# Kernel optimization log

Hardware: AMD Instinct MI355X
Metric: run time of the kernel (lower is better)

## Reference

```python
import jax, jax.numpy as jnp
import numpy as np

B, T, C, H, L, V = 512, 128, 512, 8, 6, 13
D = C // H  # 64


def setup_inputs() -> dict:
    key = jax.random.key(0)
    ks = jax.random.split(key, 12)
    s = 0.02
    return {
        "token_idxs": jax.random.randint(ks[0], (B, T), 0, V),
        "label": jax.random.randint(ks[1], (B,), 0, V),
        "wte": jax.random.normal(ks[2], (V, C), jnp.float32) * s,
        "wpe": jax.random.normal(ks[3], (T, C), jnp.float32) * s,
        "Wq": jax.random.normal(ks[4], (L, C, C), jnp.float32) * s,
        "bq": jnp.zeros((L, C), jnp.float32),
        "Wk": jax.random.normal(ks[5], (L, C, C), jnp.float32) * s,
        "bk": jnp.zeros((L, C), jnp.float32),
        "Wv": jax.random.normal(ks[6], (L, C, C), jnp.float32) * s,
        "bv": jnp.zeros((L, C), jnp.float32),
        "Wo": jax.random.normal(ks[7], (L, C, C), jnp.float32) * s,
        "bo": jnp.zeros((L, C), jnp.float32),
        "ln_g": jnp.ones((L, C), jnp.float32),
        "ln_b": jnp.zeros((L, C), jnp.float32),
        "W_lm": jax.random.normal(ks[8], (C, V), jnp.float32) * s,
        "b_lm": jnp.zeros((V,), jnp.float32),
    }


def _layer_norm(x, g, b, eps=1e-5):
    m = jnp.mean(x, axis=-1, keepdims=True)
    v = jnp.var(x, axis=-1, keepdims=True)
    return (x - m) / jnp.sqrt(v + eps) * g + b


def reference(token_idxs, label, wte, wpe, Wq, bq, Wk, bk, Wv, bv, Wo, bo, ln_g, ln_b, W_lm, b_lm):
    b, t = token_idxs.shape
    x = wte[token_idxs] + wpe[jnp.arange(t)]  # [b,t,C]
    inv_sqrt_d = 1.0 / jnp.sqrt(jnp.float32(D))
    for i in range(L):
        q = (x @ Wq[i] + bq[i]).reshape(b, t, H, D)
        k = (x @ Wk[i] + bk[i]).reshape(b, t, H, D)
        v = (x @ Wv[i] + bv[i]).reshape(b, t, H, D)
        # NOTE: matches the source exactly: attention over the HEAD axis at
        # each (b,t) position -> att shape [b,t,H,H]
        att = jnp.einsum('bthd,btgd->bthg', q, k) * inv_sqrt_d
        att = jax.nn.softmax(att, axis=-1)
        hid = jnp.einsum('bthg,btgd->bthd', att, v).reshape(b, t, C)
        x = _layer_norm(hid @ Wo[i] + bo[i] + x, ln_g[i], ln_b[i])
    logits = x @ W_lm + b_lm  # [b,t,V]
    logp = jax.nn.log_softmax(logits[:, -1, :], axis=-1)
    loss = -jnp.take_along_axis(logp, label[:, None], axis=-1).mean()
    return logits, loss
```

## Files before the change

kernel.cpp:

```cpp
#include <hip/hip_runtime.h>
#include <hip/hip_bf16.h>
#include <cstdint>
#include <cstddef>


typedef __attribute__((ext_vector_type(8))) short short8;
typedef __attribute__((ext_vector_type(4))) float f32x4;

__device__ __forceinline__ float bf2f(ushort u) {
    return __uint_as_float(((unsigned int)u) << 16);
}
__device__ __forceinline__ ushort f2bf(float f) {
    unsigned int x = __float_as_uint(f);
    unsigned int r = (x + 0x7fffu + ((x >> 16) & 1u)) >> 16;
    return (ushort)r;
}
__device__ __forceinline__ void gload_lds16(const void* g, void* l) {
    __builtin_amdgcn_global_load_lds(
        (const __attribute__((address_space(1))) void*)g,
        (__attribute__((address_space(3))) void*)l, 16, 0, 0);
}

__global__ __launch_bounds__(256) void prep_all(
    const float* __restrict__ Wq, const float* __restrict__ Wk,
    const float* __restrict__ Wv, const float* __restrict__ Wo,
    const float* __restrict__ wte, const float* __restrict__ wpe,
    const float* __restrict__ ln_g, const float* __restrict__ ln_b,
    ushort* __restrict__ wqkvT, ushort* __restrict__ woT,
    ushort* __restrict__ tmp0, float* __restrict__ s_qkv,
    float* __restrict__ t_qkv, float* __restrict__ psA,
    float* __restrict__ pssA, float* __restrict__ ones,
    float* __restrict__ zeros) {
    __shared__ float lds[64][65];
    __shared__ float gld[64], bld[64];
    __shared__ float sred[4][64], tred[4][64];
    const int bid = blockIdx.x;
    const int tid = threadIdx.x;
    if (bid < 192) {
        const int mat = bid >> 3;
        const int tc = bid & 7;
        const int l = mat >> 2, which = mat & 3;
        const float* S;
        switch (which) {
            case 0: S = Wq; break;
            case 1: S = Wk; break;
            case 2: S = Wv; break;
            default: S = Wo; break;
        }
        S += (size_t)l * 262144;
        ushort* T = (which < 3) ? wqkvT + (size_t)l * 786432 + which * 262144
                                : woT + (size_t)l * 262144;
        const bool fold = (which < 3);
        const float* g = (fold && l > 0) ? ln_g + (l - 1) * 512 : nullptr;
        const float* b = (fold && l > 0) ? ln_b + (l - 1) * 512 : nullptr;
        const int c = tid & 63;
        float sp = 0.f, tp = 0.f;
        for (int tr = 0; tr < 8; tr++) {
            __syncthreads();
            #pragma unroll
            for (int it = 0; it < 16; it++) {
                int r = it * 4 + (tid >> 6);
                lds[r][c] = S[(size_t)(tr * 64 + r) * 512 + tc * 64 + c];
            }
            if (tid < 64) {
                gld[tid] = g ? g[tr * 64 + tid] : 1.f;
                bld[tid] = b ? b[tr * 64 + tid] : 0.f;
            }
            __syncthreads();
            float gk = fold ? gld[c] : 1.f;
            #pragma unroll
            for (int it = 0; it < 16; it++) {
                int rn = it * 4 + (tid >> 6);
                float val = lds[c][rn] * gk;
                T[(size_t)(tc * 64 + rn) * 512 + tr * 64 + c] = f2bf(val);
            }
            if (fold) {
                #pragma unroll
                for (int i = 0; i < 16; i++) {
                    int kl = (tid >> 6) * 16 + i;
                    float w = lds[kl][c];
                    sp += gld[kl] * w;
                    tp += bld[kl] * w;
                }
            }
        }
        if (fold) {
            __syncthreads();
            sred[tid >> 6][c] = sp;
            tred[tid >> 6][c] = tp;
            __syncthreads();
            if (tid < 64) {
                float ss = sred[0][tid] + sred[1][tid] + sred[2][tid] + sred[3][tid];
                float tt = tred[0][tid] + tred[1][tid] + tred[2][tid] + tred[3][tid];
                int o = l * 1536 + which * 512 + tc * 64 + tid;
                s_qkv[o] = ss;
                t_qkv[o] = tt;
            }
        }
    } else if (bid < 608) {
        size_t idx = (size_t)(bid - 192) * 256 + tid;
        size_t u = idx >> 6;
        int c8 = (int)(idx & 63);
        int v = (int)(u >> 7);
        int t = (int)(u & 127);
        const float* ep = wte + (size_t)v * 512 + c8 * 8;
        const float* pp = wpe + (size_t)t * 512 + c8 * 8;
        float4 e0 = *(const float4*)ep, e1 = *(const float4*)(ep + 4);
        float4 p0 = *(const float4*)pp, p1 = *(const float4*)(pp + 4);
        float s[8] = {e0.x + p0.x, e0.y + p0.y, e0.z + p0.z, e0.w + p0.w,
                      e1.x + p1.x, e1.y + p1.y, e1.z + p1.z, e1.w + p1.w};
        short8 o;
        #pragma unroll
        for (int j = 0; j < 8; j++) o[j] = (short)f2bf(s[j]);
        *(short8*)(tmp0 + u * 512 + c8 * 8) = o;
    } else if (bid < 660) {
        int i = (bid - 608) * 256 + tid;
        if (i < 6656) psA[i] = 0.f;
        else {
            int j = i - 6656;
            pssA[j] = (j < 1664) ? 511.99488f : 0.f;
        }
    } else {
        ones[tid] = 1.f;  ones[tid + 256] = 1.f;
        zeros[tid] = 0.f; zeros[tid + 256] = 0.f;
    }
}

__global__ __launch_bounds__(256) void qkv_fold(
    const ushort* __restrict__ A, const float* __restrict__ psin,
    const float* __restrict__ pssin, const ushort* __restrict__ Bt,
    const float* __restrict__ s_l, const float* __restrict__ t_l,
    const float* __restrict__ b0, const float* __restrict__ b1,
    const float* __restrict__ b2, ushort* __restrict__ obf) {
    __shared__ alignas(16) ushort As[2][32 * 64];
    __shared__ alignas(16) ushort Bs[2][128 * 64];
    __shared__ float smu[32], srs[32];
    const int tid = threadIdx.x;
    const int lane = tid & 63;
    const int wave = tid >> 6;
    const int m0 = blockIdx.x * 32;
    const int n0 = blockIdx.y * 128;
    const int wm = (wave >> 1) * 16;
    const int wn = (wave & 1) * 64;
    const int r = lane & 15;
    const int kq = (lane >> 4) * 8;
    const ushort* Ab = A  + (size_t)m0 * 512;
    const ushort* Bb = Bt + (size_t)n0 * 512;
    f32x4 acc[4] = {};

    auto stage = [&](int t, int b) {
        const ushort* At = Ab + t * 64;
        const ushort* Bt2 = Bb + t * 64;
        {
            int cb = wave * 64;
            int ch = cb + lane;
            int row = ch >> 3;
            int c8 = (ch & 7) ^ (row & 7);
            gload_lds16(At + (size_t)row * 512 + c8 * 8, (char*)As[b] + cb * 16);
        }
        #pragma unroll
        for (int i = 0; i < 4; i++) {
            int cb = (i * 4 + wave) * 64;
            int ch = cb + lane;
            int row = ch >> 3;
            int c8 = (ch & 7) ^ (row & 7);
            gload_lds16(Bt2 + (size_t)row * 512 + c8 * 8, (char*)Bs[b] + cb * 16);
        }
    };

    stage(0, 0);
    if (tid < 32) {
        int row = m0 + tid;
        float s  = psin[row] + psin[1664 + row] + psin[3328 + row] + psin[4992 + row];
        float ss = pssin[row] + pssin[1664 + row] + pssin[3328 + row] + pssin[4992 + row];
        float mean = s * (1.f / 512.f);
        float var = ss * (1.f / 512.f) - mean * mean;
        smu[tid] = mean;
        srs[tid] = rsqrtf(var + 1e-5f);
    }
    __syncthreads();
    #pragma unroll
    for (int t = 0; t < 8; t++) {
        const int cur = t & 1;
        if (t < 7) stage(t + 1, cur ^ 1);
        #pragma unroll
        for (int kk = 0; kk < 64; kk += 32) {
            int arow = wm + r;
            int aoff = (arow * 128 + (kk + kq) * 2) ^ ((arow & 7) << 4);
            short8 af = *(const short8*)((const char*)As[cur] + aoff);
            #pragma unroll
            for (int n = 0; n < 4; n++) {
                int brow = wn + n * 16 + r;
                int boff = (brow * 128 + (kk + kq) * 2) ^ ((brow & 7) << 4);
                short8 bfr = *(const short8*)((const char*)Bs[cur] + boff);
                acc[n] = __builtin_amdgcn_mfma_f32_16x16x32_bf16(
                    af, bfr, acc[n], 0, 0, 0);
            }
        }
        __syncthreads();
    }
    const int r4 = (lane >> 4) * 4;
    const int cc = lane & 15;
    #pragma unroll
    for (int n = 0; n < 4; n++) {
        int cg = n0 + wn + n * 16 + cc;
        float bias = (cg < 512) ? b0[cg] : (cg < 1024) ? b1[cg - 512] : b2[cg - 1024];
        float sc = s_l[cg];
        float tc_ = t_l[cg] + bias;
        #pragma unroll
        for (int i = 0; i < 4; i++) {
            int lrow = wm + r4 + i;
            float v = srs[lrow] * (acc[n][i] - smu[lrow] * sc) + tc_;
            obf[(size_t)(m0 + lrow) * 1536 + cg] = f2bf(v);
        }
    }
}

__global__ __launch_bounds__(256) void attn_kernel(const ushort* __restrict__ qkv,
                                                   ushort* __restrict__ hid) {
    const int lane = threadIdx.x & 63;
    const size_t pos = (size_t)blockIdx.x * 4 + (threadIdx.x >> 6);
    const ushort* base = qkv + pos * 1536;
    const int h = lane >> 3, g = lane & 7;
    const ushort* qp = base + h * 64;
    const ushort* kp = base + 512 + g * 64;
    float s = 0.f;
    #pragma unroll
    for (int dc = 0; dc < 8; dc++) {
        short8 q8 = *(const short8*)(qp + dc * 8);
        short8 k8 = *(const short8*)(kp + dc * 8);
        #pragma unroll
        for (int j = 0; j < 8; j++) s += bf2f((ushort)q8[j]) * bf2f((ushort)k8[j]);
    }
    s *= 0.125f;
    float mx = s;
    #pragma unroll
    for (int o = 1; o < 8; o <<= 1) mx = fmaxf(mx, __shfl_xor(mx, o));
    float e = __expf(s - mx);
    float den = e;
    #pragma unroll
    for (int o = 1; o < 8; o <<= 1) den += __shfl_xor(den, o);
    float att = e / den;
    float o8[8];
    #pragma unroll
    for (int j = 0; j < 8; j++) o8[j] = 0.f;
    const ushort* vp = base + 1024 + (lane & 7) * 8;
    #pragma unroll
    for (int gg = 0; gg < 8; gg++) {
        float a = __shfl(att, (lane & 56) | gg);
        short8 v8 = *(const short8*)(vp + gg * 64);
        #pragma unroll
        for (int j = 0; j < 8; j++) o8[j] += a * bf2f((ushort)v8[j]);
    }
    short8 ov;
    #pragma unroll
    for (int j = 0; j < 8; j++) ov[j] = (short)f2bf(o8[j]);
    *(short8*)(hid + pos * 512 + lane * 8) = ov;
}

__global__ __launch_bounds__(256) void proj_fold(
    const ushort* __restrict__ A, const ushort* __restrict__ Bt,
    const float* __restrict__ bo_, const float* __restrict__ psin,
    const float* __restrict__ pssin, const float* __restrict__ g_in,
    const float* __restrict__ b_in, ushort* tmp,
    float* __restrict__ psout, float* __restrict__ pssout) {
    __shared__ alignas(16) ushort As[2][32 * 64];
    __shared__ alignas(16) ushort Bs[2][128 * 64];
    __shared__ float lps[2][32], lpss[2][32];
    __shared__ float smu[32], srs[32];
    const int tid = threadIdx.x;
    const int lane = tid & 63;
    const int wave = tid >> 6;
    const int m0 = blockIdx.x * 32;
    const int n0 = blockIdx.y * 128;
    const int wm = (wave >> 1) * 16;
    const int wn = (wave & 1) * 64;
    const int r = lane & 15;
    const int kq = (lane >> 4) * 8;
    const ushort* Ab = A  + (size_t)m0 * 512;
    const ushort* Bb = Bt + (size_t)n0 * 512;
    f32x4 acc[4] = {};

    auto stage = [&](int t, int b) {
        const ushort* At = Ab + t * 64;
        const ushort* Bt2 = Bb + t * 64;
        {
            int cb = wave * 64;
            int ch = cb + lane;
            int row = ch >> 3;
            int c8 = (ch & 7) ^ (row & 7);
            gload_lds16(At + (size_t)row * 512 + c8 * 8, (char*)As[b] + cb * 16);
        }
        #pragma unroll
        for (int i = 0; i < 4; i++) {
            int cb = (i * 4 + wave) * 64;
            int ch = cb + lane;
            int row = ch >> 3;
            int c8 = (ch & 7) ^ (row & 7);
            gload_lds16(Bt2 + (size_t)row * 512 + c8 * 8, (char*)Bs[b] + cb * 16);
        }
    };

    stage(0, 0);
    if (tid < 32) {
        int row = m0 + tid;
        float s  = psin[row] + psin[1664 + row] + psin[3328 + row] + psin[4992 + row];
        float ss = pssin[row] + pssin[1664 + row] + pssin[3328 + row] + pssin[4992 + row];
        float mean = s * (1.f / 512.f);
        float var = ss * (1.f / 512.f) - mean * mean;
        smu[tid] = mean;
        srs[tid] = rsqrtf(var + 1e-5f);
    }
    __syncthreads();
    #pragma unroll
    for (int t = 0; t < 8; t++) {
        const int cur = t & 1;
        if (t < 7) stage(t + 1, cur ^ 1);
        #pragma unroll
        for (int kk = 0; kk < 64; kk += 32) {
            int arow = wm + r;
            int aoff = (arow * 128 + (kk + kq) * 2) ^ ((arow & 7) << 4);
            short8 af = *(const short8*)((const char*)As[cur] + aoff);
            #pragma unroll
            for (int n = 0; n < 4; n++) {
                int brow = wn + n * 16 + r;
                int boff = (brow * 128 + (kk + kq) * 2) ^ ((brow & 7) << 4);
                short8 bfr = *(const short8*)((const char*)Bs[cur] + boff);
                acc[n] = __builtin_amdgcn_mfma_f32_16x16x32_bf16(
                    af, bfr, acc[n], 0, 0, 0);
            }
        }
        __syncthreads();
    }

    const int r4 = (lane >> 4) * 4;
    const int cc = lane & 15;
    float s_i[4] = {0.f, 0.f, 0.f, 0.f}, ss_i[4] = {0.f, 0.f, 0.f, 0.f};
    #pragma unroll
    for (int n = 0; n < 4; n++) {
        int col = n0 + wn + n * 16 + cc;
        float boc = bo_[col];
        float gc = g_in[col], bc = b_in[col];
        #pragma unroll
        for (int i = 0; i < 4; i++) {
            int lr = wm + r4 + i;
            int rg = m0 + lr;
            float resid = (bf2f(tmp[(size_t)rg * 512 + col]) - smu[lr])
                          * srs[lr] * gc + bc;
            float v = acc[n][i] + boc + resid;
            tmp[(size_t)rg * 512 + col] = f2bf(v);
            s_i[i] += v; ss_i[i] += v * v;
        }
    }
    #pragma unroll
    for (int i = 0; i < 4; i++) {
        #pragma unroll
        for (int o = 1; o < 16; o <<= 1) {
            s_i[i] += __shfl_xor(s_i[i], o);
            ss_i[i] += __shfl_xor(ss_i[i], o);
        }
    }
    if (cc == 0) {
        #pragma unroll
        for (int i = 0; i < 4; i++) {
            lps[wn >> 6][wm + r4 + i] = s_i[i];
            lpss[wn >> 6][wm + r4 + i] = ss_i[i];
        }
    }
    __syncthreads();
    if (tid < 32) {
        int row = m0 + tid;
        psout[blockIdx.y * 1664 + row]  = lps[0][tid] + lps[1][tid];
        pssout[blockIdx.y * 1664 + row] = lpss[0][tid] + lpss[1][tid];
    }
}

__global__ __launch_bounds__(256) void logits_ln(
    const ushort* __restrict__ tin, const float* __restrict__ psin,
    const float* __restrict__ pssin, const float* __restrict__ gv,
    const float* __restrict__ bv, const float* __restrict__ Wlm,
    const float* __restrict__ blm, float* __restrict__ lu) {
    __shared__ float wl[8 * 64 * 13];
    const int tid = threadIdx.x;
    for (int k = tid; k < 512; k += 256) {
        int dst = ((k & 7) * 64 + (k >> 3)) * 13;
        #pragma unroll
        for (int v = 0; v < 13; v++) wl[dst + v] = Wlm[k * 13 + v];
    }
    __syncthreads();
    const int lane = tid & 63;
    const int w = tid >> 6;
    const int c0 = lane * 8;
    float4 g0 = *(const float4*)(gv + c0), g1 = *(const float4*)(gv + c0 + 4);
    float4 b0 = *(const float4*)(bv + c0), b1 = *(const float4*)(bv + c0 + 4);
    float gg[8] = {g0.x, g0.y, g0.z, g0.w, g1.x, g1.y, g1.z, g1.w};
    float bb[8] = {b0.x, b0.y, b0.z, b0.w, b1.x, b1.y, b1.z, b1.w};
    float bl[13];
    #pragma unroll
    for (int v = 0; v < 13; v++) bl[v] = blm[v];
    for (int it = 0; it < 8; it++) {
        size_t row = (size_t)blockIdx.x * 32 + it * 4 + w;
        float s  = psin[row] + psin[1664 + row] + psin[3328 + row] + psin[4992 + row];
        float ss = pssin[row] + pssin[1664 + row] + pssin[3328 + row] + pssin[4992 + row];
        float mean = s * (1.f / 512.f);
        float rstd = rsqrtf(ss * (1.f / 512.f) - mean * mean + 1e-5f);
        short8 xv = *(const short8*)(tin + row * 512 + c0);
        float p[13];
        #pragma unroll
        for (int v = 0; v < 13; v++) p[v] = 0.f;
        #pragma unroll
        for (int j = 0; j < 8; j++) {
            float xf = (bf2f((ushort)xv[j]) - mean) * rstd * gg[j] + bb[j];
            const float* wr = wl + (j * 64 + lane) * 13;
            #pragma unroll
            for (int v = 0; v < 13; v++) p[v] += xf * wr[v];
        }
        #pragma unroll
        for (int v = 0; v < 13; v++) {
            #pragma unroll
            for (int o = 32; o > 0; o >>= 1) p[v] += __shfl_xor(p[v], o);
        }
        if (lane == 0) {
            #pragma unroll
            for (int v = 0; v < 13; v++) lu[row * 13 + v] = p[v] + bl[v];
        }
    }
}

__global__ __launch_bounds__(256) void scatter_loss(
    const float* __restrict__ lu, const int* __restrict__ tok,
    const int* __restrict__ label, float* __restrict__ out) {
    __shared__ float red[4];
    const int tid = threadIdx.x;
    if (blockIdx.x < 3328) {
        unsigned int i = blockIdx.x * 256 + tid;
        unsigned int bt = i / 13u;
        unsigned int vv = i - bt * 13u;
        int v = tok[bt];
        int t = (int)(bt & 127u);
        out[i] = lu[(size_t)((v << 7) + t) * 13 + vv];
    } else {
        float acc = 0.f;
        for (int b = tid; b < 512; b += 256) {
            int v = tok[b * 128 + 127];
            const float* lg = lu + (size_t)((v << 7) + 127) * 13;
            float mx = lg[0];
            #pragma unroll
            for (int vv = 1; vv < 13; vv++) mx = fmaxf(mx, lg[vv]);
            float den = 0.f;
            #pragma unroll
            for (int vv = 0; vv < 13; vv++) den += expf(lg[vv] - mx);
            int lab = label[b];
            acc += -(lg[lab] - mx - logf(den));
        }
        #pragma unroll
        for (int o = 32; o > 0; o >>= 1) acc += __shfl_xor(acc, o);
        if ((tid & 63) == 0) red[tid >> 6] = acc;
        __syncthreads();
        if (tid == 0)
            out[851968] = (red[0] + red[1] + red[2] + red[3]) * (1.f / 512.f);
    }
}

extern "C" void kernel_launch(void* const* d_in, const int* in_sizes, int n_in,
                              void* d_out, int out_size, void* d_ws, size_t ws_size,
                              hipStream_t stream) {
    const int*   tok   = (const int*)d_in[0];
    const int*   label = (const int*)d_in[1];
    const float* wte   = (const float*)d_in[2];
    const float* wpe   = (const float*)d_in[3];
    const float* Wq    = (const float*)d_in[4];
    const float* bq    = (const float*)d_in[5];
    const float* Wk    = (const float*)d_in[6];
    const float* bk    = (const float*)d_in[7];
    const float* Wv    = (const float*)d_in[8];
    const float* bv    = (const float*)d_in[9];
    const float* Wo    = (const float*)d_in[10];
    const float* bo    = (const float*)d_in[11];
    const float* ln_g  = (const float*)d_in[12];
    const float* ln_b  = (const float*)d_in[13];
    const float* Wlm   = (const float*)d_in[14];
    const float* blm   = (const float*)d_in[15];
    float* out = (float*)d_out;

    char* ws = (char*)d_ws;
    ushort* wqkvT = (ushort*)(ws);
    ushort* woT   = (ushort*)(ws + 9437184);
    ushort* qkv_u = (ushort*)(ws + 12582912);
    ushort* hid_u = (ushort*)(ws + 17694720);
    ushort* tmp   = (ushort*)(ws + 19398656);
    float*  psA   = (float*) (ws + 21102592);
    float*  pssA  = (float*) (ws + 21129216);
    float*  psB   = (float*) (ws + 21155840);
    float*  pssB  = (float*) (ws + 21182464);
    float*  lu    = (float*) (ws + 21209088);
    float*  s_qkv = (float*) (ws + 21295616);
    float*  t_qkv = (float*) (ws + 21332480);
    float*  ones  = (float*) (ws + 21369344);
    float*  zeros = (float*) (ws + 21371392);

    prep_all<<<661, 256, 0, stream>>>(Wq, Wk, Wv, Wo, wte, wpe, ln_g, ln_b,
                                      wqkvT, woT, tmp, s_qkv, t_qkv,
                                      psA, pssA, ones, zeros);

    const float *psin = psA, *pssin = pssA;
    float *psout = psB, *pssout = pssB;
    for (int l = 0; l < 6; l++) {
        const float* g_in = (l == 0) ? ones  : ln_g + (l - 1) * 512;
        const float* b_in = (l == 0) ? zeros : ln_b + (l - 1) * 512;
        qkv_fold<<<dim3(52, 12), 256, 0, stream>>>(
            tmp, psin, pssin, wqkvT + (size_t)l * 786432,
            s_qkv + l * 1536, t_qkv + l * 1536,
            bq + l * 512, bk + l * 512, bv + l * 512, qkv_u);
        attn_kernel<<<416, 256, 0, stream>>>(qkv_u, hid_u);
        proj_fold<<<dim3(52, 4), 256, 0, stream>>>(
            hid_u, woT + (size_t)l * 262144, bo + l * 512,
            psin, pssin, g_in, b_in, tmp, psout, pssout);
        const float* p1 = psin;  psin = psout;  psout = (float*)p1;
        const float* p2 = pssin; pssin = pssout; pssout = (float*)p2;
    }

    logits_ln<<<52, 256, 0, stream>>>(tmp, psin, pssin,
                                      ln_g + 5 * 512, ln_b + 5 * 512, Wlm, blm, lu);
    scatter_loss<<<3329, 256, 0, stream>>>(lu, tok, label, out);
}
```

Measured before the change: 221.5 us.

## Split weight prep into per-tile transpose blocks and separate fold-reduction blocks

The prep kernel previously had 192 blocks, each looping over 8 row-tiles to transpose a 64-column strip while also accumulating the LayerNorm fold sums. It now launches one block per 64x64 tile for the transpose (1536 blocks) and a separate set of 144 blocks that read the weights directly to compute the s/t fold vectors. The goal is to expose far more parallelism in the prep phase and cut its serial latency. The cost is that the fold blocks re-read the fp32 weights from global memory with strided loads, and the block-index ranges are reordered.

```diff
diff --git a/kernel.cpp b/kernel.cpp
--- a/kernel.cpp
+++ b/kernel.cpp
@@ -31,14 +31,13 @@
     float* __restrict__ t_qkv, float* __restrict__ psA,
     float* __restrict__ pssA, float* __restrict__ ones,
     float* __restrict__ zeros) {
-    __shared__ float lds[64][65];
-    __shared__ float gld[64], bld[64];
-    __shared__ float sred[4][64], tred[4][64];
     const int bid = blockIdx.x;
     const int tid = threadIdx.x;
-    if (bid < 192) {
-        const int mat = bid >> 3;
-        const int tc = bid & 7;
+    if (bid < 1536) {
+        __shared__ float lds[64][65];
+        const int mat = bid >> 6;
+        const int tile = bid & 63;
+        const int tr = tile >> 3, tc = tile & 7;
         const int l = mat >> 2, which = mat & 3;
         const float* S;
         switch (which) {
@@ -50,55 +49,53 @@
         S += (size_t)l * 262144;
         ushort* T = (which < 3) ? wqkvT + (size_t)l * 786432 + which * 262144
                                 : woT + (size_t)l * 262144;
-        const bool fold = (which < 3);
-        const float* g = (fold && l > 0) ? ln_g + (l - 1) * 512 : nullptr;
-        const float* b = (fold && l > 0) ? ln_b + (l - 1) * 512 : nullptr;
         const int c = tid & 63;
+        #pragma unroll
+        for (int it = 0; it < 16; it++) {
+            int r = it * 4 + (tid >> 6);
+            lds[r][c] = S[(size_t)(tr * 64 + r) * 512 + tc * 64 + c];
+        }
+        float gk = 1.f;
+        if (which < 3 && l > 0) gk = ln_g[(l - 1) * 512 + tr * 64 + c];
+        __syncthreads();
+        #pragma unroll
+        for (int it = 0; it < 16; it++) {
+            int r = it * 4 + (tid >> 6);
+            T[(size_t)(tc * 64 + r) * 512 + tr * 64 + c] = f2bf(lds[c][r] * gk);
+        }
+    } else if (bid < 1680) {
+        __shared__ float sred[4][64], tred[4][64];
+        const int j = bid - 1536;
+        const int mat = j >> 3;
+        const int tc = j & 7;
+        const int l = mat / 3, which = mat % 3;
+        const float* S = (which == 0) ? Wq : (which == 1) ? Wk : Wv;
+        S += (size_t)l * 262144;
+        const float* g = (l > 0) ? ln_g + (l - 1) * 512 : nullptr;
+        const float* b = (l > 0) ? ln_b + (l - 1) * 512 : nullptr;
+        const int c = tid & 63;
+        const int kc = tid >> 6;
         float sp = 0.f, tp = 0.f;
-        for (int tr = 0; tr < 8; tr++) {
-            __syncthreads();
-            #pragma unroll
-            for (int it = 0; it < 16; it++) {
-                int r = it * 4 + (tid >> 6);
-                lds[r][c] = S[(size_t)(tr * 64 + r) * 512 + tc * 64 + c];
-            }
-            if (tid < 64) {
-                gld[tid] = g ? g[tr * 64 + tid] : 1.f;
-                bld[tid] = b ? b[tr * 64 + tid] : 0.f;
-            }
-            __syncthreads();
-            float gk = fold ? gld[c] : 1.f;
-            #pragma unroll
-            for (int it = 0; it < 16; it++) {
-                int rn = it * 4 + (tid >> 6);
-                float val = lds[c][rn] * gk;
-                T[(size_t)(tc * 64 + rn) * 512 + tr * 64 + c] = f2bf(val);
-            }
-            if (fold) {
-                #pragma unroll
-                for (int i = 0; i < 16; i++) {
-                    int kl = (tid >> 6) * 16 + i;
-                    float w = lds[kl][c];
-                    sp += gld[kl] * w;
-                    tp += bld[kl] * w;
-                }
-            }
-        }
-        if (fold) {
-            __syncthreads();
-            sred[tid >> 6][c] = sp;
-            tred[tid >> 6][c] = tp;
-            __syncthreads();
-            if (tid < 64) {
-                float ss = sred[0][tid] + sred[1][tid] + sred[2][tid] + sred[3][tid];
-                float tt = tred[0][tid] + tred[1][tid] + tred[2][tid] + tred[3][tid];
-                int o = l * 1536 + which * 512 + tc * 64 + tid;
-                s_qkv[o] = ss;
-                t_qkv[o] = tt;
-            }
-        }
-    } else if (bid < 608) {
-        size_t idx = (size_t)(bid - 192) * 256 + tid;
+        for (int ki = 0; ki < 128; ki++) {
+            int k = kc * 128 + ki;
+            float w = S[(size_t)k * 512 + tc * 64 + c];
+            float gv = g ? g[k] : 1.f;
+            float bv = b ? b[k] : 0.f;
+            sp += gv * w;
+            tp += bv * w;
+        }
+        sred[kc][c] = sp;
+        tred[kc][c] = tp;
+        __syncthreads();
+        if (tid < 64) {
+            float ss = sred[0][tid] + sred[1][tid] + sred[2][tid] + sred[3][tid];
+            float tt = tred[0][tid] + tred[1][tid] + tred[2][tid] + tred[3][tid];
+            int o = l * 1536 + which * 512 + tc * 64 + tid;
+            s_qkv[o] = ss;
+            t_qkv[o] = tt;
+        }
+    } else if (bid < 2096) {
+        size_t idx = (size_t)(bid - 1680) * 256 + tid;
         size_t u = idx >> 6;
         int c8 = (int)(idx & 63);
         int v = (int)(u >> 7);
@@ -113,16 +110,16 @@
         #pragma unroll
         for (int j = 0; j < 8; j++) o[j] = (short)f2bf(s[j]);
         *(short8*)(tmp0 + u * 512 + c8 * 8) = o;
-    } else if (bid < 660) {
-        int i = (bid - 608) * 256 + tid;
+    } else if (bid == 2096) {
+        ones[tid] = 1.f;  ones[tid + 256] = 1.f;
+        zeros[tid] = 0.f; zeros[tid + 256] = 0.f;
+    } else {
+        int i = (bid - 2097) * 256 + tid;
         if (i < 6656) psA[i] = 0.f;
         else {
             int j = i - 6656;
             pssA[j] = (j < 1664) ? 511.99488f : 0.f;
         }
-    } else {
-        ones[tid] = 1.f;  ones[tid + 256] = 1.f;
-        zeros[tid] = 0.f; zeros[tid + 256] = 0.f;
     }
 }
 
@@ -499,9 +496,9 @@
     float*  ones  = (float*) (ws + 21369344);
     float*  zeros = (float*) (ws + 21371392);
 
-    prep_all<<<661, 256, 0, stream>>>(Wq, Wk, Wv, Wo, wte, wpe, ln_g, ln_b,
-                                      wqkvT, woT, tmp, s_qkv, t_qkv,
-                                      psA, pssA, ones, zeros);
+    prep_all<<<2149, 256, 0, stream>>>(Wq, Wk, Wv, Wo, wte, wpe, ln_g, ln_b,
+                                       wqkvT, woT, tmp, s_qkv, t_qkv,
+                                       psA, pssA, ones, zeros);
 
     const float *psin = psA, *pssin = pssA;
     float *psout = psB, *pssout = pssB;
```

Measured after the change: 223.9 us. Within noise of the previous version (+1.1%).
